# Kernel tuning notes

Measured on AMD Instinct MI355X. Metric: run time of the kernel, lower is better.

The kernel has to match this reference:

```python
import math
import jax, jax.numpy as jnp
import numpy as np

NUM_HEADS = 12
KEEP_RATE = 0.7


def setup_inputs() -> dict:
    key = jax.random.key(0)
    k1, k2, k3 = jax.random.split(key, 3)
    B, N, C = 16, 577, 768
    x = jax.random.normal(k1, (B, N, C), dtype=jnp.float32)
    qkv_w = jax.random.normal(k2, (3 * C, C), dtype=jnp.float32) * 0.02
    proj_w = jax.random.normal(k3, (C, C), dtype=jnp.float32) * 0.02
    proj_b = jnp.zeros((C,), dtype=jnp.float32)
    return {"x": x, "qkv_w": qkv_w, "proj_w": proj_w, "proj_b": proj_b}


def reference(x, qkv_w, proj_w, proj_b):
    B, N, C = x.shape
    H = NUM_HEADS
    hd = C // H
    scale = hd ** -0.5
    # qkv projection (no bias): [B, N, 3C] -> [3, B, H, N, hd]
    qkv = (x @ qkv_w.T).reshape(B, N, 3, H, hd).transpose(2, 0, 3, 1, 4)
    q, k, v = qkv[0], qkv[1], qkv[2]
    attn = jax.nn.softmax(jnp.einsum('bhnd,bhmd->bhnm', q, k) * scale, axis=-1)
    out = jnp.einsum('bhnm,bhmd->bhnd', attn, v)          # [B,H,N,hd]
    out = out.transpose(0, 2, 1, 3).reshape(B, N, C)
    out = out @ proj_w.T + proj_b
    # CLS-token attention pruning (keep_rate < 1.0, return_idx=True path)
    left_tokens = math.ceil(KEEP_RATE * (N - 1))
    cls_attn = attn[:, :, 0, 1:].mean(axis=1)             # [B, N-1], mean over heads
    _, idx = jax.lax.top_k(cls_attn, left_tokens)         # sorted descending
    index = jnp.broadcast_to(idx[:, :, None], (B, left_tokens, C))
    return out, idx, index, cls_attn
```

## Files before the change

kernel.cpp:

```cpp
#include <hip/hip_runtime.h>
#include <math.h>

#define BB 16
#define NN 577
#define CC 768
#define HH 12
#define HD 64
#define MM (BB*NN)
#define MPAD 9344
#define LEFT 404
#define NPAD 608
#define NQT 10

typedef __attribute__((ext_vector_type(8))) short short8v;
typedef __attribute__((ext_vector_type(4))) float f32x4;

__device__ __forceinline__ unsigned short f2bf(float f) {
    union { float f; unsigned int u; } v; v.f = f;
    unsigned int r = v.u + 0x7fffu + ((v.u >> 16) & 1u);
    return (unsigned short)(r >> 16);
}

__global__ __launch_bounds__(256) void k_gemm_fp32(const float* __restrict__ X,
                                                   const float* __restrict__ W,
                                                   float* __restrict__ kb,
                                                   unsigned short* __restrict__ kbh)
{
    __shared__ float Xs[16][128];
    __shared__ float Ws[16][128];
    const int t  = threadIdx.x;
    const int tx = t & 15, ty = t >> 4;
    const int m0 = blockIdx.x * 128;
    const int n0 = 768 + blockIdx.y * 128;
    const int sm = t & 127;
    const int sk = (t >> 7) * 8;

    float acc[8][8];
    #pragma unroll
    for (int i = 0; i < 8; ++i)
        #pragma unroll
        for (int j = 0; j < 8; ++j) acc[i][j] = 0.f;

    for (int kk = 0; kk < CC; kk += 16) {
        {
            const int gm = m0 + sm;
            float4 a0 = make_float4(0.f,0.f,0.f,0.f), a1 = a0;
            if (gm < MM) {
                const float* p = X + (size_t)gm * CC + kk + sk;
                a0 = *(const float4*)p;
                a1 = *(const float4*)(p + 4);
            }
            Xs[sk+0][sm] = a0.x; Xs[sk+1][sm] = a0.y; Xs[sk+2][sm] = a0.z; Xs[sk+3][sm] = a0.w;
            Xs[sk+4][sm] = a1.x; Xs[sk+5][sm] = a1.y; Xs[sk+6][sm] = a1.z; Xs[sk+7][sm] = a1.w;
            const float* pw = W + (size_t)(n0 + sm) * CC + kk + sk;
            float4 b0 = *(const float4*)pw;
            float4 b1 = *(const float4*)(pw + 4);
            Ws[sk+0][sm] = b0.x; Ws[sk+1][sm] = b0.y; Ws[sk+2][sm] = b0.z; Ws[sk+3][sm] = b0.w;
            Ws[sk+4][sm] = b1.x; Ws[sk+5][sm] = b1.y; Ws[sk+6][sm] = b1.z; Ws[sk+7][sm] = b1.w;
        }
        __syncthreads();
        #pragma unroll
        for (int k = 0; k < 16; ++k) {
            float a[8], bv[8];
            *(float4*)&a[0]  = *(const float4*)&Xs[k][ty*8];
            *(float4*)&a[4]  = *(const float4*)&Xs[k][ty*8+4];
            *(float4*)&bv[0] = *(const float4*)&Ws[k][tx*8];
            *(float4*)&bv[4] = *(const float4*)&Ws[k][tx*8+4];
            #pragma unroll
            for (int i = 0; i < 8; ++i)
                #pragma unroll
                for (int j = 0; j < 8; ++j)
                    acc[i][j] = fmaf(a[i], bv[j], acc[i][j]);
        }
        __syncthreads();
    }
    #pragma unroll
    for (int i = 0; i < 8; ++i) {
        const int gm = m0 + ty*8 + i;
        if (gm >= MM) continue;
        const int b_ = gm / NN;
        const int n_ = gm - b_ * NN;
        #pragma unroll
        for (int j = 0; j < 8; ++j) {
            const int col = n0 + tx*8 + j - 768;
            const int h = col >> 6, d = col & 63;
            const float a = acc[i][j];
            kb [(((size_t)b_ * HH + h) * NN   + n_) * HD + d] = a;
            kbh[(((size_t)b_ * HH + h) * NPAD + n_) * HD + d] = f2bf(a);
        }
    }
}

__global__ __launch_bounds__(256) void qcls_kernel(const float* __restrict__ X,
                                                   const float* __restrict__ W,
                                                   float* __restrict__ qcls)
{
    const int b = blockIdx.x;
    const int col = blockIdx.y * 256 + threadIdx.x;
    const float* xr = X + (size_t)b * NN * CC;
    const float* wr = W + (size_t)col * CC;
    float acc = 0.f;
    for (int k = 0; k < CC; ++k) acc = fmaf(xr[k], wr[k], acc);
    qcls[(size_t)b * CC + col] = acc;
}

#define N4X 1772544
#define N4W 442368
#define N4P 147456
__global__ __launch_bounds__(256) void convert3(const float* __restrict__ x,
                                                const float* __restrict__ wq,
                                                const float* __restrict__ wp,
                                                unsigned short* __restrict__ xb,
                                                unsigned short* __restrict__ wqb,
                                                unsigned short* __restrict__ wpb)
{
    int g = blockIdx.x * 256 + threadIdx.x;
    const float* src; unsigned short* dst;
    if (g < N4X)            { src = x;  dst = xb;  }
    else if (g < N4X + N4W) { g -= N4X; src = wq; dst = wqb; }
    else                    { g -= (N4X + N4W); src = wp; dst = wpb; }
    const float4 v = ((const float4*)src)[g];
    ushort4 o;
    o.x = f2bf(v.x); o.y = f2bf(v.y); o.z = f2bf(v.z); o.w = f2bf(v.w);
    ((ushort4*)dst)[g] = o;
}

__global__ __launch_bounds__(256) void qv_mfma(const unsigned short* __restrict__ xbh,
                                               const unsigned short* __restrict__ wqkv,
                                               unsigned short* __restrict__ qbh,
                                               unsigned short* __restrict__ Vt)
{
    __shared__ unsigned short As[128*32];
    __shared__ unsigned short Bs[128*32];
    const int t = threadIdx.x;
    const int w = t >> 6, l = t & 63;
    const int l15 = l & 15, lk = l >> 4;
    const int wm = w >> 1, wn = w & 1;
    const int m0 = blockIdx.x * 128;
    const int isV = blockIdx.y >= 6;
    const int nlocal0 = (isV ? (blockIdx.y - 6) : blockIdx.y) * 128;
    const int wrow0 = (isV ? 1536 : 0) + nlocal0;
    const int r0 = t >> 2, segp = t & 3;

    f32x4 acc[4][4];
    #pragma unroll
    for (int i = 0; i < 4; ++i)
        #pragma unroll
        for (int j = 0; j < 4; ++j) acc[i][j] = (f32x4){0.f,0.f,0.f,0.f};

    const unsigned short* ga = xbh  + (size_t)(m0 + r0) * CC + segp * 8;
    const unsigned short* gb = wqkv + (size_t)(wrow0 + r0) * CC + segp * 8;

    for (int kk = 0; kk < CC; kk += 32) {
        const short8v a0 = *(const short8v*)(ga + kk);
        const short8v a1 = *(const short8v*)(ga + kk + (size_t)64 * CC);
        const short8v b0 = *(const short8v*)(gb + kk);
        const short8v b1 = *(const short8v*)(gb + kk + (size_t)64 * CC);
        __syncthreads();
        *(short8v*)&As[(r0)      * 32 + segp*8] = a0;
        *(short8v*)&As[(64 + r0) * 32 + segp*8] = a1;
        *(short8v*)&Bs[(r0)      * 32 + segp*8] = b0;
        *(short8v*)&Bs[(64 + r0) * 32 + segp*8] = b1;
        __syncthreads();
        short8v fa[4], fb[4];
        #pragma unroll
        for (int i = 0; i < 4; ++i) fa[i] = *(const short8v*)&As[(wm*64 + i*16 + l15)*32 + lk*8];
        #pragma unroll
        for (int j = 0; j < 4; ++j) fb[j] = *(const short8v*)&Bs[(wn*64 + j*16 + l15)*32 + lk*8];
        #pragma unroll
        for (int i = 0; i < 4; ++i)
            #pragma unroll
            for (int j = 0; j < 4; ++j)
                acc[i][j] = __builtin_amdgcn_mfma_f32_16x16x32_bf16(fa[i], fb[j], acc[i][j], 0, 0, 0);
    }

    const int nb = nlocal0 + wn*64 + l15;
    #pragma unroll
    for (int i = 0; i < 4; ++i) {
        #pragma unroll
        for (int r = 0; r < 4; ++r) {
            const int m = m0 + wm*64 + i*16 + 4*lk + r;
            if (m >= MM) continue;
            const int b_ = m / NN, tok = m - b_ * NN;
            #pragma unroll
            for (int j = 0; j < 4; ++j) {
                const int nl = nb + j*16;
                const int h = nl >> 6, d = nl & 63;
                const unsigned short v = f2bf(acc[i][j][r]);
                if (isV) Vt [(((size_t)b_*HH + h)*HD + d)*NPAD + tok] = v;
                else     qbh[(((size_t)b_*HH + h)*NPAD + tok)*HD + d] = v;
            }
        }
    }
}

__global__ __launch_bounds__(256) void proj_mfma(const unsigned short* __restrict__ aobh,
                                                 const unsigned short* __restrict__ wpb,
                                                 const float* __restrict__ bias,
                                                 float* __restrict__ outp)
{
    __shared__ unsigned short As[128*32];
    __shared__ unsigned short Bs[128*32];
    const int t = threadIdx.x;
    const int w = t >> 6, l = t & 63;
    const int l15 = l & 15, lk = l >> 4;
    const int wm = w >> 1, wn = w & 1;
    const int m0 = blockIdx.x * 128;
    const int n0 = blockIdx.y * 128;
    const int r0 = t >> 2, segp = t & 3;

    f32x4 acc[4][4];
    #pragma unroll
    for (int i = 0; i < 4; ++i)
        #pragma unroll
        for (int j = 0; j < 4; ++j) acc[i][j] = (f32x4){0.f,0.f,0.f,0.f};

    const unsigned short* ga = aobh + (size_t)(m0 + r0) * CC + segp * 8;
    const unsigned short* gb = wpb  + (size_t)(n0 + r0) * CC + segp * 8;

    for (int kk = 0; kk < CC; kk += 32) {
        const short8v a0 = *(const short8v*)(ga + kk);
        const short8v a1 = *(const short8v*)(ga + kk + (size_t)64 * CC);
        const short8v b0 = *(const short8v*)(gb + kk);
        const short8v b1 = *(const short8v*)(gb + kk + (size_t)64 * CC);
        __syncthreads();
        *(short8v*)&As[(r0)      * 32 + segp*8] = a0;
        *(short8v*)&As[(64 + r0) * 32 + segp*8] = a1;
        *(short8v*)&Bs[(r0)      * 32 + segp*8] = b0;
        *(short8v*)&Bs[(64 + r0) * 32 + segp*8] = b1;
        __syncthreads();
        short8v fa[4], fb[4];
        #pragma unroll
        for (int i = 0; i < 4; ++i) fa[i] = *(const short8v*)&As[(wm*64 + i*16 + l15)*32 + lk*8];
        #pragma unroll
        for (int j = 0; j < 4; ++j) fb[j] = *(const short8v*)&Bs[(wn*64 + j*16 + l15)*32 + lk*8];
        #pragma unroll
        for (int i = 0; i < 4; ++i)
            #pragma unroll
            for (int j = 0; j < 4; ++j)
                acc[i][j] = __builtin_amdgcn_mfma_f32_16x16x32_bf16(fa[i], fb[j], acc[i][j], 0, 0, 0);
    }

    const int nb = n0 + wn*64 + l15;
    #pragma unroll
    for (int i = 0; i < 4; ++i) {
        #pragma unroll
        for (int r = 0; r < 4; ++r) {
            const int m = m0 + wm*64 + i*16 + 4*lk + r;
            if (m >= MM) continue;
            #pragma unroll
            for (int j = 0; j < 4; ++j) {
                const int n = nb + j*16;
                outp[(size_t)m * CC + n] = acc[i][j][r] + bias[n];
            }
        }
    }
}

__global__ __launch_bounds__(256) void attn_mfma(const unsigned short* __restrict__ qbh,
                                                 const unsigned short* __restrict__ kbh,
                                                 const unsigned short* __restrict__ Vt,
                                                 unsigned short* __restrict__ aobh)
{
    __shared__ __align__(16) unsigned short plds[4][16][32];
    const int bid = blockIdx.x;
    const int bh  = bid / NQT;
    const int qt  = bid - bh * NQT;
    const int b   = bh / HH, h = bh - b * HH;
    const int t   = threadIdx.x;
    const int w   = t >> 6, l = t & 63;
    const int l15 = l & 15, lg = l >> 4;

    short8v aq0, aq1;
    {
        int qrow = qt*64 + w*16 + l15; if (qrow > 576) qrow = 576;
        const unsigned short* qp = qbh + ((size_t)bh * NPAD + qrow) * HD + lg*8;
        aq0 = *(const short8v*)(qp);
        aq1 = *(const short8v*)(qp + 32);
    }

    f32x4 O0 = {0.f,0.f,0.f,0.f}, O1 = O0, O2 = O0, O3 = O0;
    float mr[4] = {-1e30f,-1e30f,-1e30f,-1e30f};
    float lr[4] = {0.f,0.f,0.f,0.f};

    const unsigned short* kwb = kbh + (size_t)bh * NPAD * HD + (size_t)l15 * HD + lg*8;
    const unsigned short* vwb = Vt  + (size_t)bh * HD * NPAD + (size_t)l15 * NPAD + lg*8;

    for (int c = 0; c < 19; ++c) {
        const int n0 = c * 32;
        const unsigned short* kp = kwb + (size_t)n0 * HD;
        short8v bk00 = *(const short8v*)(kp);
        short8v bk01 = *(const short8v*)(kp + 32);
        short8v bk10 = *(const short8v*)(kp + 16*HD);
        short8v bk11 = *(const short8v*)(kp + 16*HD + 32);
        f32x4 s0 = {0.f,0.f,0.f,0.f}, s1 = {0.f,0.f,0.f,0.f};
        s0 = __builtin_amdgcn_mfma_f32_16x16x32_bf16(aq0, bk00, s0, 0, 0, 0);
        s0 = __builtin_amdgcn_mfma_f32_16x16x32_bf16(aq1, bk01, s0, 0, 0, 0);
        s1 = __builtin_amdgcn_mfma_f32_16x16x32_bf16(aq0, bk10, s1, 0, 0, 0);
        s1 = __builtin_amdgcn_mfma_f32_16x16x32_bf16(aq1, bk11, s1, 0, 0, 0);

        const int nc0 = n0 + l15;
        float p0[4], p1[4], al[4];
        #pragma unroll
        for (int r = 0; r < 4; ++r) {
            float a0 = (nc0      <= 576) ? s0[r] * 0.125f : -1e30f;
            float a1 = (nc0 + 16 <= 576) ? s1[r] * 0.125f : -1e30f;
            float tm = fmaxf(a0, a1);
            tm = fmaxf(tm, __shfl_xor(tm, 1, 64));
            tm = fmaxf(tm, __shfl_xor(tm, 2, 64));
            tm = fmaxf(tm, __shfl_xor(tm, 4, 64));
            tm = fmaxf(tm, __shfl_xor(tm, 8, 64));
            const float mn = fmaxf(mr[r], tm);
            al[r] = __expf(mr[r] - mn);
            mr[r] = mn;
            p0[r] = __expf(a0 - mn);
            p1[r] = __expf(a1 - mn);
            float ps = p0[r] + p1[r];
            ps += __shfl_xor(ps, 1, 64);
            ps += __shfl_xor(ps, 2, 64);
            ps += __shfl_xor(ps, 4, 64);
            ps += __shfl_xor(ps, 8, 64);
            lr[r] = lr[r] * al[r] + ps;
        }
        #pragma unroll
        for (int r = 0; r < 4; ++r) {
            O0[r] *= al[r]; O1[r] *= al[r]; O2[r] *= al[r]; O3[r] *= al[r];
        }
        #pragma unroll
        for (int r = 0; r < 4; ++r) {
            plds[w][lg*4 + r][l15]      = f2bf(p0[r]);
            plds[w][lg*4 + r][16 + l15] = f2bf(p1[r]);
        }
        asm volatile("s_waitcnt lgkmcnt(0)" ::: "memory");
        short8v pa = *(const short8v*)&plds[w][l15][lg*8];
        const unsigned short* vp = vwb + n0;
        short8v v0 = *(const short8v*)(vp);
        short8v v1 = *(const short8v*)(vp + 16*NPAD);
        short8v v2 = *(const short8v*)(vp + 32*NPAD);
        short8v v3 = *(const short8v*)(vp + 48*NPAD);
        O0 = __builtin_amdgcn_mfma_f32_16x16x32_bf16(pa, v0, O0, 0, 0, 0);
        O1 = __builtin_amdgcn_mfma_f32_16x16x32_bf16(pa, v1, O1, 0, 0, 0);
        O2 = __builtin_amdgcn_mfma_f32_16x16x32_bf16(pa, v2, O2, 0, 0, 0);
        O3 = __builtin_amdgcn_mfma_f32_16x16x32_bf16(pa, v3, O3, 0, 0, 0);
    }

    #pragma unroll
    for (int r = 0; r < 4; ++r) {
        const float inv = 1.f / lr[r];
        const int row = qt*64 + w*16 + lg*4 + r;
        if (row <= 576) {
            unsigned short* op = aobh + ((size_t)b * NN + row) * CC + h*HD + l15;
            op[0]  = f2bf(O0[r] * inv);
            op[16] = f2bf(O1[r] * inv);
            op[32] = f2bf(O2[r] * inv);
            op[48] = f2bf(O3[r] * inv);
        }
    }
}

__global__ __launch_bounds__(256) void cls_scores(const float* __restrict__ qcls,
                                                  const float* __restrict__ kb,
                                                  float* __restrict__ P)
{
    const int bh = blockIdx.x;
    const int t = threadIdx.x;
    __shared__ float q[64];
    __shared__ float red[256];
    __shared__ float L[NN];
    if (t < 64) q[t] = qcls[(size_t)bh * 64 + t];
    __syncthreads();
    float lmax = -1e30f;
    for (int n = t; n < NN; n += 256) {
        const float* kr = kb + ((size_t)bh * NN + n) * HD;
        float acc = 0.f;
        #pragma unroll
        for (int d = 0; d < 64; ++d) acc = fmaf(q[d], kr[d], acc);
        const float l = acc * 0.125f;
        L[n] = l;
        lmax = fmaxf(lmax, l);
    }
    red[t] = lmax; __syncthreads();
    for (int s = 128; s > 0; s >>= 1) { if (t < s) red[t] = fmaxf(red[t], red[t+s]); __syncthreads(); }
    const float m = red[0]; __syncthreads();
    float z = 0.f;
    for (int n = t; n < NN; n += 256) { const float e = expf(L[n] - m); L[n] = e; z += e; }
    red[t] = z; __syncthreads();
    for (int s = 128; s > 0; s >>= 1) { if (t < s) red[t] += red[t+s]; __syncthreads(); }
    const float Z = red[0];
    for (int n = t; n < NN; n += 256) P[(size_t)bh * NN + n] = L[n] / Z;
}

__global__ __launch_bounds__(256) void cls_mean32(const float* __restrict__ P,
                                                  float* __restrict__ cls32,
                                                  float* __restrict__ out_cls)
{
    const int b = blockIdx.x;
    for (int j = threadIdx.x; j < NN - 1; j += 256) {
        float s = 0.f;
        #pragma unroll
        for (int h = 0; h < HH; ++h) s += P[((size_t)(b * HH + h)) * NN + 1 + j];
        const float v = s / 12.0f;
        cls32[b * 576 + j] = v;
        out_cls[b * 576 + j] = v;
    }
}

__global__ __launch_bounds__(256) void topk_rank(const float* __restrict__ cls32,
                                                 float* __restrict__ out_idx,
                                                 int* __restrict__ idxi)
{
    const int b = blockIdx.x;
    const int t = threadIdx.x;
    __shared__ float sv[576];
    for (int i = t; i < 576; i += 256) sv[i] = cls32[b * 576 + i];
    __syncthreads();
    for (int i = t; i < 576; i += 256) {
        const float vi = sv[i];
        int rank = 0;
        for (int j = 0; j < 576; ++j) {
            const float vj = sv[j];
            if (vj > vi || (vj == vi && j < i)) ++rank;
        }
        if (rank < LEFT) {
            out_idx[(size_t)b * LEFT + rank] = (float)i;
            idxi[(size_t)b * LEFT + rank] = i;
        }
    }
}

__global__ void write_index(const int* __restrict__ idxi, float* __restrict__ out_index)
{
    const int g4 = blockIdx.x * 256 + threadIdx.x;
    const float v = (float)idxi[g4 / 192];
    float4 o; o.x = v; o.y = v; o.z = v; o.w = v;
    ((float4*)out_index)[g4] = o;
}

extern "C" void kernel_launch(void* const* d_in, const int* in_sizes, int n_in,
                              void* d_out, int out_size, void* d_ws, size_t ws_size,
                              hipStream_t stream)
{
    const float* x      = (const float*)d_in[0];
    const float* qkv_w  = (const float*)d_in[1];
    const float* proj_w = (const float*)d_in[2];
    const float* proj_b = (const float*)d_in[3];
    float* out = (float*)d_out;

    char* base = (char*)d_ws;
    float*          kb    = (float*)(base + 0);
    unsigned short* xbh   = (unsigned short*)(base +  28360704);
    unsigned short* qbh   = (unsigned short*)(base +  42713088);
    unsigned short* kbh   = (unsigned short*)(base +  57655296);
    unsigned short* Vt    = (unsigned short*)(base +  72597504);
    unsigned short* aobh  = (unsigned short*)(base +  87539712);
    unsigned short* wqkv  = (unsigned short*)(base + 101892096);
    unsigned short* wpb   = (unsigned short*)(base + 105431040);
    float*          qcls  = (float*)(base + 106610688);
    float*          P     = (float*)(base + 106659840);
    float*          cls32 = (float*)(base + 107102976);
    int*            idxi  = (int*)  (base + 107139840);

    float* out_main  = out;
    float* out_idx   = out + 7090176;
    float* out_index = out + 7096640;
    float* out_cls   = out + 12060992;

    convert3<<<9228, 256, 0, stream>>>(x, qkv_w, proj_w, xbh, wqkv, wpb);
    qcls_kernel<<<dim3(16, 3), 256, 0, stream>>>(x, qkv_w, qcls);
    k_gemm_fp32<<<dim3(73, 6), 256, 0, stream>>>(x, qkv_w, kb, kbh);
    qv_mfma<<<dim3(73, 12), 256, 0, stream>>>(xbh, wqkv, qbh, Vt);
    attn_mfma<<<BB * HH * NQT, 256, 0, stream>>>(qbh, kbh, Vt, aobh);
    proj_mfma<<<dim3(73, 6), 256, 0, stream>>>(aobh, wpb, proj_b, out_main);

    cls_scores<<<BB * HH, 256, 0, stream>>>(qcls, kb, P);
    cls_mean32<<<BB, 256, 0, stream>>>(P, cls32, out_cls);
    topk_rank<<<BB, 256, 0, stream>>>(cls32, out_idx, idxi);
    write_index<<<4848, 256, 0, stream>>>(idxi, out_index);
}
```

Measured before the change: 445.8 us.

## Fuse fp32 K GEMM and bf16 Q/V MFMA GEMM into one interleaved launch

Merges the fp32 SIMT K-projection kernel and the bf16 MFMA Q/V kernel into a single launch whose blocks alternate one K tile per two Q/V tiles. The fp32 K GEMM gains register prefetching of the next k-slice and a split 4+4 thread-to-row/column mapping to reduce LDS bank conflicts. The goal is to let the slow fp32 blocks overlap with the MFMA blocks on the same CUs and to save a launch. Register pressure is now set by the heavier branch for every block, which may lower occupancy for the MFMA path.

```diff
diff --git a/kernel.cpp b/kernel.cpp
--- a/kernel.cpp
+++ b/kernel.cpp
@@ -21,72 +21,147 @@
     return (unsigned short)(r >> 16);
 }
 
-__global__ __launch_bounds__(256) void k_gemm_fp32(const float* __restrict__ X,
-                                                   const float* __restrict__ W,
-                                                   float* __restrict__ kb,
-                                                   unsigned short* __restrict__ kbh)
-{
-    __shared__ float Xs[16][128];
-    __shared__ float Ws[16][128];
-    const int t  = threadIdx.x;
-    const int tx = t & 15, ty = t >> 4;
-    const int m0 = blockIdx.x * 128;
-    const int n0 = 768 + blockIdx.y * 128;
-    const int sm = t & 127;
-    const int sk = (t >> 7) * 8;
-
-    float acc[8][8];
-    #pragma unroll
-    for (int i = 0; i < 8; ++i)
-        #pragma unroll
-        for (int j = 0; j < 8; ++j) acc[i][j] = 0.f;
-
-    for (int kk = 0; kk < CC; kk += 16) {
-        {
-            const int gm = m0 + sm;
-            float4 a0 = make_float4(0.f,0.f,0.f,0.f), a1 = a0;
-            if (gm < MM) {
-                const float* p = X + (size_t)gm * CC + kk + sk;
-                a0 = *(const float4*)p;
-                a1 = *(const float4*)(p + 4);
-            }
+__global__ __launch_bounds__(256) void k_qv_fused(const float* __restrict__ X,
+                                                  const float* __restrict__ W,
+                                                  float* __restrict__ kb,
+                                                  unsigned short* __restrict__ kbh,
+                                                  const unsigned short* __restrict__ xbh,
+                                                  const unsigned short* __restrict__ wqkv,
+                                                  unsigned short* __restrict__ qbh,
+                                                  unsigned short* __restrict__ Vt)
+{
+    __shared__ __align__(16) char smem[16384];
+    const int bid = blockIdx.x;
+    const int t = threadIdx.x;
+
+    if (bid % 3 == 0) {
+        const int kidx = bid / 3;
+        float (*Xs)[128] = (float(*)[128])smem;
+        float (*Ws)[128] = (float(*)[128])(smem + 8192);
+        const int tx = t & 15, ty = t >> 4;
+        const int m0 = (kidx % 73) * 128;
+        const int n0 = 768 + (kidx / 73) * 128;
+        const int sm = t & 127;
+        const int sk = (t >> 7) * 8;
+
+        float acc[8][8];
+        #pragma unroll
+        for (int i = 0; i < 8; ++i)
+            #pragma unroll
+            for (int j = 0; j < 8; ++j) acc[i][j] = 0.f;
+
+        const int gm = m0 + sm;
+        const float* px = X + (size_t)gm * CC + sk;
+        const float* pw = W + (size_t)(n0 + sm) * CC + sk;
+
+        float4 a0 = make_float4(0.f,0.f,0.f,0.f), a1 = a0, b0, b1;
+        if (gm < MM) { a0 = *(const float4*)px; a1 = *(const float4*)(px + 4); }
+        b0 = *(const float4*)pw; b1 = *(const float4*)(pw + 4);
+
+        for (int kk = 0; kk < CC; kk += 16) {
             Xs[sk+0][sm] = a0.x; Xs[sk+1][sm] = a0.y; Xs[sk+2][sm] = a0.z; Xs[sk+3][sm] = a0.w;
             Xs[sk+4][sm] = a1.x; Xs[sk+5][sm] = a1.y; Xs[sk+6][sm] = a1.z; Xs[sk+7][sm] = a1.w;
-            const float* pw = W + (size_t)(n0 + sm) * CC + kk + sk;
-            float4 b0 = *(const float4*)pw;
-            float4 b1 = *(const float4*)(pw + 4);
             Ws[sk+0][sm] = b0.x; Ws[sk+1][sm] = b0.y; Ws[sk+2][sm] = b0.z; Ws[sk+3][sm] = b0.w;
             Ws[sk+4][sm] = b1.x; Ws[sk+5][sm] = b1.y; Ws[sk+6][sm] = b1.z; Ws[sk+7][sm] = b1.w;
-        }
-        __syncthreads();
-        #pragma unroll
-        for (int k = 0; k < 16; ++k) {
-            float a[8], bv[8];
-            *(float4*)&a[0]  = *(const float4*)&Xs[k][ty*8];
-            *(float4*)&a[4]  = *(const float4*)&Xs[k][ty*8+4];
-            *(float4*)&bv[0] = *(const float4*)&Ws[k][tx*8];
-            *(float4*)&bv[4] = *(const float4*)&Ws[k][tx*8+4];
-            #pragma unroll
-            for (int i = 0; i < 8; ++i)
+            __syncthreads();
+            if (kk + 16 < CC) {
+                a0 = make_float4(0.f,0.f,0.f,0.f); a1 = a0;
+                if (gm < MM) { a0 = *(const float4*)(px + kk + 16); a1 = *(const float4*)(px + kk + 20); }
+                b0 = *(const float4*)(pw + kk + 16); b1 = *(const float4*)(pw + kk + 20);
+            }
+            #pragma unroll
+            for (int k = 0; k < 16; ++k) {
+                float a[8], bv[8];
+                *(float4*)&a[0]  = *(const float4*)&Xs[k][ty*4];
+                *(float4*)&a[4]  = *(const float4*)&Xs[k][64 + ty*4];
+                *(float4*)&bv[0] = *(const float4*)&Ws[k][tx*4];
+                *(float4*)&bv[4] = *(const float4*)&Ws[k][64 + tx*4];
                 #pragma unroll
-                for (int j = 0; j < 8; ++j)
-                    acc[i][j] = fmaf(a[i], bv[j], acc[i][j]);
-        }
-        __syncthreads();
-    }
-    #pragma unroll
-    for (int i = 0; i < 8; ++i) {
-        const int gm = m0 + ty*8 + i;
-        if (gm >= MM) continue;
-        const int b_ = gm / NN;
-        const int n_ = gm - b_ * NN;
-        #pragma unroll
-        for (int j = 0; j < 8; ++j) {
-            const int col = n0 + tx*8 + j - 768;
-            const int h = col >> 6, d = col & 63;
-            const float a = acc[i][j];
-            kb [(((size_t)b_ * HH + h) * NN   + n_) * HD + d] = a;
-            kbh[(((size_t)b_ * HH + h) * NPAD + n_) * HD + d] = f2bf(a);
+                for (int i = 0; i < 8; ++i)
+                    #pragma unroll
+                    for (int j = 0; j < 8; ++j)
+                        acc[i][j] = fmaf(a[i], bv[j], acc[i][j]);
+            }
+            __syncthreads();
+        }
+        #pragma unroll
+        for (int i = 0; i < 8; ++i) {
+            const int mrow = m0 + ((i < 4) ? (ty*4 + i) : (64 + ty*4 + i - 4));
+            if (mrow >= MM) continue;
+            const int b_ = mrow / NN;
+            const int n_ = mrow - b_ * NN;
+            #pragma unroll
+            for (int j = 0; j < 8; ++j) {
+                const int col = (n0 - 768) + ((j < 4) ? (tx*4 + j) : (64 + tx*4 + j - 4));
+                const int h = col >> 6, d = col & 63;
+                const float a = acc[i][j];
+                kb [(((size_t)b_ * HH + h) * NN   + n_) * HD + d] = a;
+                kbh[(((size_t)b_ * HH + h) * NPAD + n_) * HD + d] = f2bf(a);
+            }
+        }
+    } else {
+        const int qbid = (bid / 3) * 2 + (bid % 3) - 1;
+        unsigned short* As = (unsigned short*)smem;
+        unsigned short* Bs = (unsigned short*)(smem + 8192);
+        const int w = t >> 6, l = t & 63;
+        const int l15 = l & 15, lk = l >> 4;
+        const int wm = w >> 1, wn = w & 1;
+        const int m0 = (qbid % 73) * 128;
+        const int by = qbid / 73;
+        const int isV = by >= 6;
+        const int nlocal0 = (isV ? (by - 6) : by) * 128;
+        const int wrow0 = (isV ? 1536 : 0) + nlocal0;
+        const int r0 = t >> 2, segp = t & 3;
+
+        f32x4 acc[4][4];
+        #pragma unroll
+        for (int i = 0; i < 4; ++i)
+            #pragma unroll
+            for (int j = 0; j < 4; ++j) acc[i][j] = (f32x4){0.f,0.f,0.f,0.f};
+
+        const unsigned short* ga = xbh  + (size_t)(m0 + r0) * CC + segp * 8;
+        const unsigned short* gb = wqkv + (size_t)(wrow0 + r0) * CC + segp * 8;
+
+        for (int kk = 0; kk < CC; kk += 32) {
+            const short8v a0 = *(const short8v*)(ga + kk);
+            const short8v a1 = *(const short8v*)(ga + kk + (size_t)64 * CC);
+            const short8v b0 = *(const short8v*)(gb + kk);
+            const short8v b1 = *(const short8v*)(gb + kk + (size_t)64 * CC);
+            __syncthreads();
+            *(short8v*)&As[(r0)      * 32 + segp*8] = a0;
+            *(short8v*)&As[(64 + r0) * 32 + segp*8] = a1;
+            *(short8v*)&Bs[(r0)      * 32 + segp*8] = b0;
+            *(short8v*)&Bs[(64 + r0) * 32 + segp*8] = b1;
+            __syncthreads();
+            short8v fa[4], fb[4];
+            #pragma unroll
+            for (int i = 0; i < 4; ++i) fa[i] = *(const short8v*)&As[(wm*64 + i*16 + l15)*32 + lk*8];
+            #pragma unroll
+            for (int j = 0; j < 4; ++j) fb[j] = *(const short8v*)&Bs[(wn*64 + j*16 + l15)*32 + lk*8];
+            #pragma unroll
+            for (int i = 0; i < 4; ++i)
+                #pragma unroll
+                for (int j = 0; j < 4; ++j)
+                    acc[i][j] = __builtin_amdgcn_mfma_f32_16x16x32_bf16(fa[i], fb[j], acc[i][j], 0, 0, 0);
+        }
+
+        const int nb = nlocal0 + wn*64 + l15;
+        #pragma unroll
+        for (int i = 0; i < 4; ++i) {
+            #pragma unroll
+            for (int r = 0; r < 4; ++r) {
+                const int m = m0 + wm*64 + i*16 + 4*lk + r;
+                if (m >= MM) continue;
+                const int b_ = m / NN, tok = m - b_ * NN;
+                #pragma unroll
+                for (int j = 0; j < 4; ++j) {
+                    const int nl = nb + j*16;
+                    const int h = nl >> 6, d = nl & 63;
+                    const unsigned short v = f2bf(acc[i][j][r]);
+                    if (isV) Vt [(((size_t)b_*HH + h)*HD + d)*NPAD + tok] = v;
+                    else     qbh[(((size_t)b_*HH + h)*NPAD + tok)*HD + d] = v;
+                }
+            }
         }
     }
 }
@@ -123,75 +198,6 @@
     ushort4 o;
     o.x = f2bf(v.x); o.y = f2bf(v.y); o.z = f2bf(v.z); o.w = f2bf(v.w);
     ((ushort4*)dst)[g] = o;
-}
-
-__global__ __launch_bounds__(256) void qv_mfma(const unsigned short* __restrict__ xbh,
-                                               const unsigned short* __restrict__ wqkv,
-                                               unsigned short* __restrict__ qbh,
-                                               unsigned short* __restrict__ Vt)
-{
-    __shared__ unsigned short As[128*32];
-    __shared__ unsigned short Bs[128*32];
-    const int t = threadIdx.x;
-    const int w = t >> 6, l = t & 63;
-    const int l15 = l & 15, lk = l >> 4;
-    const int wm = w >> 1, wn = w & 1;
-    const int m0 = blockIdx.x * 128;
-    const int isV = blockIdx.y >= 6;
-    const int nlocal0 = (isV ? (blockIdx.y - 6) : blockIdx.y) * 128;
-    const int wrow0 = (isV ? 1536 : 0) + nlocal0;
-    const int r0 = t >> 2, segp = t & 3;
-
-    f32x4 acc[4][4];
-    #pragma unroll
-    for (int i = 0; i < 4; ++i)
-        #pragma unroll
-        for (int j = 0; j < 4; ++j) acc[i][j] = (f32x4){0.f,0.f,0.f,0.f};
-
-    const unsigned short* ga = xbh  + (size_t)(m0 + r0) * CC + segp * 8;
-    const unsigned short* gb = wqkv + (size_t)(wrow0 + r0) * CC + segp * 8;
-
-    for (int kk = 0; kk < CC; kk += 32) {
-        const short8v a0 = *(const short8v*)(ga + kk);
-        const short8v a1 = *(const short8v*)(ga + kk + (size_t)64 * CC);
-        const short8v b0 = *(const short8v*)(gb + kk);
-        const short8v b1 = *(const short8v*)(gb + kk + (size_t)64 * CC);
-        __syncthreads();
-        *(short8v*)&As[(r0)      * 32 + segp*8] = a0;
-        *(short8v*)&As[(64 + r0) * 32 + segp*8] = a1;
-        *(short8v*)&Bs[(r0)      * 32 + segp*8] = b0;
-        *(short8v*)&Bs[(64 + r0) * 32 + segp*8] = b1;
-        __syncthreads();
-        short8v fa[4], fb[4];
-        #pragma unroll
-        for (int i = 0; i < 4; ++i) fa[i] = *(const short8v*)&As[(wm*64 + i*16 + l15)*32 + lk*8];
-        #pragma unroll
-        for (int j = 0; j < 4; ++j) fb[j] = *(const short8v*)&Bs[(wn*64 + j*16 + l15)*32 + lk*8];
-        #pragma unroll
-        for (int i = 0; i < 4; ++i)
-            #pragma unroll
-            for (int j = 0; j < 4; ++j)
-                acc[i][j] = __builtin_amdgcn_mfma_f32_16x16x32_bf16(fa[i], fb[j], acc[i][j], 0, 0, 0);
-    }
-
-    const int nb = nlocal0 + wn*64 + l15;
-    #pragma unroll
-    for (int i = 0; i < 4; ++i) {
-        #pragma unroll
-        for (int r = 0; r < 4; ++r) {
-            const int m = m0 + wm*64 + i*16 + 4*lk + r;
-            if (m >= MM) continue;
-            const int b_ = m / NN, tok = m - b_ * NN;
-            #pragma unroll
-            for (int j = 0; j < 4; ++j) {
-                const int nl = nb + j*16;
-                const int h = nl >> 6, d = nl & 63;
-                const unsigned short v = f2bf(acc[i][j][r]);
-                if (isV) Vt [(((size_t)b_*HH + h)*HD + d)*NPAD + tok] = v;
-                else     qbh[(((size_t)b_*HH + h)*NPAD + tok)*HD + d] = v;
-            }
-        }
-    }
 }
 
 __global__ __launch_bounds__(256) void proj_mfma(const unsigned short* __restrict__ aobh,
@@ -467,8 +473,7 @@
 
     convert3<<<9228, 256, 0, stream>>>(x, qkv_w, proj_w, xbh, wqkv, wpb);
     qcls_kernel<<<dim3(16, 3), 256, 0, stream>>>(x, qkv_w, qcls);
-    k_gemm_fp32<<<dim3(73, 6), 256, 0, stream>>>(x, qkv_w, kb, kbh);
-    qv_mfma<<<dim3(73, 12), 256, 0, stream>>>(xbh, wqkv, qbh, Vt);
+    k_qv_fused<<<1314, 256, 0, stream>>>(x, qkv_w, kb, kbh, xbh, wqkv, qbh, Vt);
     attn_mfma<<<BB * HH * NQT, 256, 0, stream>>>(qbh, kbh, Vt, aobh);
     proj_mfma<<<dim3(73, 6), 256, 0, stream>>>(aobh, wpb, proj_b, out_main);
 
```

Measured after the change: 511.5 us. 1.15x slower.
